# Optimization experiments

Measured on AMD Instinct MI355X. Metric: run time of the kernel, lower is better.

## Reference

```python
import jax, jax.numpy as jnp
import numpy as np

B = 1_000_000  # batch of independent 3-node graphs (trajectory samples)
H = 32         # hidden_channels

# fully-connected 3-node graph with self-loops, deg=3 => D^-1/2 A D^-1/2 = ones(3,3)/3
A_NORM = jnp.full((3, 3), 1.0 / 3.0, dtype=jnp.float32)


def setup_inputs() -> dict:
    key = jax.random.key(0)
    ks = jax.random.split(key, 8)
    return {
        "x":    jax.random.normal(ks[0], (B, 3, 4), jnp.float32),
        "W1":   jax.random.normal(ks[1], (4, H), jnp.float32) * 0.3,
        "b1":   jnp.zeros((H,), jnp.float32),
        "W2":   jax.random.normal(ks[2], (H, H), jnp.float32) * 0.15,
        "b2":   jnp.zeros((H,), jnp.float32),
        "W3":   jax.random.normal(ks[3], (H, H), jnp.float32) * 0.15,
        "b3":   jnp.zeros((H,), jnp.float32),
        "W4":   jax.random.normal(ks[4], (H, H), jnp.float32) * 0.15,
        "b4":   jnp.zeros((H,), jnp.float32),
        "linW": jax.random.normal(ks[5], (1, 3), jnp.float32) * 0.3,  # torch Linear(3,1) weight [out,in]
        "linb": jnp.zeros((1,), jnp.float32),
    }


def _gcn(h, W, b):
    # GCNLayer (eval mode: dropout is identity):
    #   linear -> symmetric-normalized sum over neighbors (= mean over all 3 nodes) -> bias -> softplus
    # h: [B, 3, Fin] -> [B, 3, Fout]
    return jax.nn.softplus(jnp.einsum('ij,bjf->bif', A_NORM, h @ W) + b)


def reference(x, W1, b1, W2, b2, W3, b3, W4, b4, linW, linb):
    h = _gcn(x, W1, b1)   # [B,3,32]
    h = _gcn(h, W2, b2)
    h = _gcn(h, W3, b3)
    h = _gcn(h, W4, b4)   # [B,3,32]
    h = jnp.swapaxes(h, -2, -1)      # [B,32,3]
    return h @ linW.T + linb         # [B,32,1]
```

## Files before the change

kernel.cpp:

```cpp
#include <hip/hip_runtime.h>
#include <math.h>


#define BLK 256
#define ROWSTRIDE 36

using short8 = __attribute__((ext_vector_type(8))) short;
using f32x4  = __attribute__((ext_vector_type(4))) float;

__device__ __forceinline__ short8 as_s8(uint4 u) { return __builtin_bit_cast(short8, u); }

__device__ __forceinline__ float softplus_fast(float a) {
    return __logf(1.0f + __expf(a));
}

__device__ __forceinline__ unsigned pack_hilo(float a) {
    unsigned u  = __float_as_uint(a);
    unsigned hb = (u + 0x7fffu + ((u >> 16) & 1u)) & 0xffff0000u;
    float    r  = a - __uint_as_float(hb);
    unsigned lo = __float_as_uint(r) >> 16;
    return hb | lo;
}

__global__ __launch_bounds__(BLK, 3) void gnn_mfma(
    const float* __restrict__ x,
    const float* __restrict__ W1, const float* __restrict__ b1,
    const float* __restrict__ W2, const float* __restrict__ b2,
    const float* __restrict__ W3, const float* __restrict__ b3,
    const float* __restrict__ W4, const float* __restrict__ b4,
    const float* __restrict__ linW, const float* __restrict__ linb,
    float* __restrict__ out, int nB)
{
    __shared__ unsigned lds[4 * 64 * ROWSTRIDE];

    const int tid  = threadIdx.x;
    const int wid  = tid >> 6;
    const int lane = tid & 63;
    const int q    = lane >> 4;
    const int l16  = lane & 15;

    unsigned* myLds = lds + wid * (64 * ROWSTRIDE);
    const int sbase = blockIdx.x * BLK + wid * 64;

    const int b0 = sbase + lane;
    float xm0 = 0.f, xm1 = 0.f, xm2 = 0.f, xm3 = 0.f;
    if (b0 < nB) {
        const float4* xp = (const float4*)(x + (size_t)b0 * 12);
        float4 n0 = xp[0], n1 = xp[1], n2 = xp[2];
        const float inv3 = 1.0f / 3.0f;
        xm0 = (n0.x + n1.x + n2.x) * inv3;
        xm1 = (n0.y + n1.y + n2.y) * inv3;
        xm2 = (n0.z + n1.z + n2.z) * inv3;
        xm3 = (n0.w + n1.w + n2.w) * inv3;
    }

    {
        unsigned vp[32];
        #pragma unroll
        for (int f = 0; f < 32; ++f) {
            float a = b1[f];
            a = fmaf(xm0, W1[f],      a);
            a = fmaf(xm1, W1[32 + f], a);
            a = fmaf(xm2, W1[64 + f], a);
            a = fmaf(xm3, W1[96 + f], a);
            vp[f] = pack_hilo(softplus_fast(a));
        }
        uint4* rowp = (uint4*)(myLds + lane * ROWSTRIDE);
        #pragma unroll
        for (int d = 0; d < 8; ++d)
            rowp[d] = make_uint4(vp[4*d], vp[4*d+1], vp[4*d+2], vp[4*d+3]);
    }

    const float* Ws[3] = { W2, W3, W4 };
    const float* bs[3] = { b2, b3, b4 };
    const float s_lin = linW[0] + linW[1] + linW[2];
    const float lb    = linb[0];

    #pragma unroll
    for (int layer = 0; layer < 3; ++layer) {
        const float* __restrict__ W  = Ws[layer];
        const float* __restrict__ bL = bs[layer];

        uint4 bhi[2], blo[2];
        #pragma unroll
        for (int nt = 0; nt < 2; ++nt) {
            float w[8];
            #pragma unroll
            for (int j = 0; j < 8; ++j)
                w[j] = W[(q * 8 + j) * 32 + nt * 16 + l16];
            #pragma unroll
            for (int d = 0; d < 4; ++d) {
                unsigned u0  = __float_as_uint(w[2*d]);
                unsigned hb0 = (u0 + 0x7fffu + ((u0 >> 16) & 1u)) & 0xffff0000u;
                float    r0  = w[2*d] - __uint_as_float(hb0);
                unsigned lo0 = __float_as_uint(r0) >> 16;
                unsigned u1  = __float_as_uint(w[2*d+1]);
                unsigned hb1 = (u1 + 0x7fffu + ((u1 >> 16) & 1u)) & 0xffff0000u;
                float    r1  = w[2*d+1] - __uint_as_float(hb1);
                unsigned lo1 = __float_as_uint(r1) >> 16;
                (&bhi[nt].x)[d] = hb1 | (hb0 >> 16);
                (&blo[nt].x)[d] = (lo1 << 16) | lo0;
            }
        }
        const float bias_v0 = bL[l16];
        const float bias_v1 = bL[16 + l16];

        uint4 ahi[4], alo[4];
        #pragma unroll
        for (int mt = 0; mt < 4; ++mt) {
            const uint4* ap = (const uint4*)(myLds + (mt * 16 + l16) * ROWSTRIDE + q * 8);
            uint4 pA = ap[0], pB = ap[1];
            unsigned p[8] = { pA.x, pA.y, pA.z, pA.w, pB.x, pB.y, pB.z, pB.w };
            #pragma unroll
            for (int d = 0; d < 4; ++d) {
                (&ahi[mt].x)[d] = __builtin_amdgcn_perm(p[2*d+1], p[2*d], 0x07060302u);
                (&alo[mt].x)[d] = __builtin_amdgcn_perm(p[2*d+1], p[2*d], 0x05040100u);
            }
        }

        f32x4 acc[4][2];
        #pragma unroll
        for (int mt = 0; mt < 4; ++mt)
            #pragma unroll
            for (int nt = 0; nt < 2; ++nt) {
                f32x4 c = { 0.f, 0.f, 0.f, 0.f };
                c = __builtin_amdgcn_mfma_f32_16x16x32_bf16(as_s8(ahi[mt]), as_s8(bhi[nt]), c, 0, 0, 0);
                c = __builtin_amdgcn_mfma_f32_16x16x32_bf16(as_s8(ahi[mt]), as_s8(blo[nt]), c, 0, 0, 0);
                c = __builtin_amdgcn_mfma_f32_16x16x32_bf16(as_s8(alo[mt]), as_s8(bhi[nt]), c, 0, 0, 0);
                acc[mt][nt] = c;
            }

        if (layer < 2) {
            #pragma unroll
            for (int mt = 0; mt < 4; ++mt)
                #pragma unroll
                for (int nt = 0; nt < 2; ++nt)
                    #pragma unroll
                    for (int r = 0; r < 4; ++r) {
                        float a = acc[mt][nt][r] + (nt ? bias_v1 : bias_v0);
                        int srow = mt * 16 + q * 4 + r;
                        myLds[srow * ROWSTRIDE + nt * 16 + l16] = pack_hilo(softplus_fast(a));
                    }
        } else {
            #pragma unroll
            for (int mt = 0; mt < 4; ++mt)
                #pragma unroll
                for (int nt = 0; nt < 2; ++nt)
                    #pragma unroll
                    for (int r = 0; r < 4; ++r) {
                        float a = acc[mt][nt][r] + (nt ? bias_v1 : bias_v0);
                        float v = softplus_fast(a);
                        int srow = mt * 16 + q * 4 + r;
                        int samp = sbase + srow;
                        if (samp < nB)
                            out[(size_t)samp * 32 + nt * 16 + l16] = fmaf(s_lin, v, lb);
                    }
        }
    }
}

extern "C" void kernel_launch(void* const* d_in, const int* in_sizes, int n_in,
                              void* d_out, int out_size, void* d_ws, size_t ws_size,
                              hipStream_t stream) {
    const float* x    = (const float*)d_in[0];
    const float* W1   = (const float*)d_in[1];
    const float* b1   = (const float*)d_in[2];
    const float* W2   = (const float*)d_in[3];
    const float* b2   = (const float*)d_in[4];
    const float* W3   = (const float*)d_in[5];
    const float* b3   = (const float*)d_in[6];
    const float* W4   = (const float*)d_in[7];
    const float* b4   = (const float*)d_in[8];
    const float* linW = (const float*)d_in[9];
    const float* linb = (const float*)d_in[10];
    float* out = (float*)d_out;

    const int nB   = in_sizes[0] / 12;
    const int grid = (nB + BLK - 1) / BLK;
    gnn_mfma<<<grid, BLK, 0, stream>>>(x, W1, b1, W2, b2, W3, b3, W4, b4,
                                       linW, linb, out, nB);
}
```

Baseline: 234.3 us.

## Store activations as plain bf16 and compute softplus in log2 domain

```diff
diff --git a/kernel.cpp b/kernel.cpp
--- a/kernel.cpp
+++ b/kernel.cpp
@@ -3,26 +3,29 @@
 
 
 #define BLK 256
-#define ROWSTRIDE 36
+#define RS  20
+
+#define LOG2E 1.44269504088896340736f
+#define LN2   0.69314718055994530942f
 
 using short8 = __attribute__((ext_vector_type(8))) short;
 using f32x4  = __attribute__((ext_vector_type(4))) float;
 
 __device__ __forceinline__ short8 as_s8(uint4 u) { return __builtin_bit_cast(short8, u); }
 
-__device__ __forceinline__ float softplus_fast(float a) {
-    return __logf(1.0f + __expf(a));
+__device__ __forceinline__ unsigned bf16_rne(float a) {
+    unsigned u = __float_as_uint(a);
+    return (u + 0x7fffu + ((u >> 16) & 1u)) >> 16;
+}
+__device__ __forceinline__ unsigned pack_bf16x2(float lo, float hi) {
+    return bf16_rne(lo) | (bf16_rne(hi) << 16);
 }
 
-__device__ __forceinline__ unsigned pack_hilo(float a) {
-    unsigned u  = __float_as_uint(a);
-    unsigned hb = (u + 0x7fffu + ((u >> 16) & 1u)) & 0xffff0000u;
-    float    r  = a - __uint_as_float(hb);
-    unsigned lo = __float_as_uint(r) >> 16;
-    return hb | lo;
+__device__ __forceinline__ float softplus_log2(float t) {
+    return __builtin_amdgcn_logf(1.0f + __builtin_amdgcn_exp2f(t));
 }
 
-__global__ __launch_bounds__(BLK, 3) void gnn_mfma(
+__global__ __launch_bounds__(BLK, 3) void gnn_mfma4(
     const float* __restrict__ x,
     const float* __restrict__ W1, const float* __restrict__ b1,
     const float* __restrict__ W2, const float* __restrict__ b2,
@@ -31,7 +34,7 @@
     const float* __restrict__ linW, const float* __restrict__ linb,
     float* __restrict__ out, int nB)
 {
-    __shared__ unsigned lds[4 * 64 * ROWSTRIDE];
+    __shared__ unsigned lds[4 * 64 * RS];
 
     const int tid  = threadIdx.x;
     const int wid  = tid >> 6;
@@ -39,7 +42,7 @@
     const int q    = lane >> 4;
     const int l16  = lane & 15;
 
-    unsigned* myLds = lds + wid * (64 * ROWSTRIDE);
+    unsigned* myLds = lds + wid * (64 * RS);
     const int sbase = blockIdx.x * BLK + wid * 64;
 
     const int b0 = sbase + lane;
@@ -47,34 +50,36 @@
     if (b0 < nB) {
         const float4* xp = (const float4*)(x + (size_t)b0 * 12);
         float4 n0 = xp[0], n1 = xp[1], n2 = xp[2];
-        const float inv3 = 1.0f / 3.0f;
-        xm0 = (n0.x + n1.x + n2.x) * inv3;
-        xm1 = (n0.y + n1.y + n2.y) * inv3;
-        xm2 = (n0.z + n1.z + n2.z) * inv3;
-        xm3 = (n0.w + n1.w + n2.w) * inv3;
+        const float k = LOG2E / 3.0f;
+        xm0 = (n0.x + n1.x + n2.x) * k;
+        xm1 = (n0.y + n1.y + n2.y) * k;
+        xm2 = (n0.z + n1.z + n2.z) * k;
+        xm3 = (n0.w + n1.w + n2.w) * k;
     }
-
     {
-        unsigned vp[32];
+        float u[32];
         #pragma unroll
         for (int f = 0; f < 32; ++f) {
-            float a = b1[f];
-            a = fmaf(xm0, W1[f],      a);
-            a = fmaf(xm1, W1[32 + f], a);
-            a = fmaf(xm2, W1[64 + f], a);
-            a = fmaf(xm3, W1[96 + f], a);
-            vp[f] = pack_hilo(softplus_fast(a));
+            float t = LOG2E * b1[f];
+            t = fmaf(xm0, W1[f],      t);
+            t = fmaf(xm1, W1[32 + f], t);
+            t = fmaf(xm2, W1[64 + f], t);
+            t = fmaf(xm3, W1[96 + f], t);
+            u[f] = softplus_log2(t);
         }
-        uint4* rowp = (uint4*)(myLds + lane * ROWSTRIDE);
+        uint4* rowp = (uint4*)(myLds + lane * RS);
         #pragma unroll
-        for (int d = 0; d < 8; ++d)
-            rowp[d] = make_uint4(vp[4*d], vp[4*d+1], vp[4*d+2], vp[4*d+3]);
+        for (int d = 0; d < 4; ++d)
+            rowp[d] = make_uint4(pack_bf16x2(u[4*d + 0], u[4*d + 16]),
+                                 pack_bf16x2(u[4*d + 1], u[4*d + 17]),
+                                 pack_bf16x2(u[4*d + 2], u[4*d + 18]),
+                                 pack_bf16x2(u[4*d + 3], u[4*d + 19]));
     }
 
     const float* Ws[3] = { W2, W3, W4 };
     const float* bs[3] = { b2, b3, b4 };
-    const float s_lin = linW[0] + linW[1] + linW[2];
-    const float lb    = linb[0];
+    const float s_lin_ln2 = (linW[0] + linW[1] + linW[2]) * LN2;
+    const float lb        = linb[0];
 
     #pragma unroll
     for (int layer = 0; layer < 3; ++layer) {
@@ -84,39 +89,24 @@
         uint4 bhi[2], blo[2];
         #pragma unroll
         for (int nt = 0; nt < 2; ++nt) {
-            float w[8];
-            #pragma unroll
-            for (int j = 0; j < 8; ++j)
-                w[j] = W[(q * 8 + j) * 32 + nt * 16 + l16];
             #pragma unroll
             for (int d = 0; d < 4; ++d) {
-                unsigned u0  = __float_as_uint(w[2*d]);
-                unsigned hb0 = (u0 + 0x7fffu + ((u0 >> 16) & 1u)) & 0xffff0000u;
-                float    r0  = w[2*d] - __uint_as_float(hb0);
-                unsigned lo0 = __float_as_uint(r0) >> 16;
-                unsigned u1  = __float_as_uint(w[2*d+1]);
-                unsigned hb1 = (u1 + 0x7fffu + ((u1 >> 16) & 1u)) & 0xffff0000u;
-                float    r1  = w[2*d+1] - __uint_as_float(hb1);
-                unsigned lo1 = __float_as_uint(r1) >> 16;
-                (&bhi[nt].x)[d] = hb1 | (hb0 >> 16);
-                (&blo[nt].x)[d] = (lo1 << 16) | lo0;
+                float w0 = W[(q * 4 + d) * 32      + nt * 16 + l16];
+                float w1 = W[(q * 4 + d + 16) * 32 + nt * 16 + l16];
+                unsigned h0 = bf16_rne(w0), h1 = bf16_rne(w1);
+                float w0h = __uint_as_float(h0 << 16);
+                float w1h = __uint_as_float(h1 << 16);
+                (&bhi[nt].x)[d] = h0 | (h1 << 16);
+                (&blo[nt].x)[d] = pack_bf16x2(w0 - w0h, w1 - w1h);
             }
         }
-        const float bias_v0 = bL[l16];
-        const float bias_v1 = bL[16 + l16];
+        const float bias0 = LOG2E * bL[l16];
+        const float bias1 = LOG2E * bL[16 + l16];
 
-        uint4 ahi[4], alo[4];
+        uint4 afr[4];
         #pragma unroll
-        for (int mt = 0; mt < 4; ++mt) {
-            const uint4* ap = (const uint4*)(myLds + (mt * 16 + l16) * ROWSTRIDE + q * 8);
-            uint4 pA = ap[0], pB = ap[1];
-            unsigned p[8] = { pA.x, pA.y, pA.z, pA.w, pB.x, pB.y, pB.z, pB.w };
-            #pragma unroll
-            for (int d = 0; d < 4; ++d) {
-                (&ahi[mt].x)[d] = __builtin_amdgcn_perm(p[2*d+1], p[2*d], 0x07060302u);
-                (&alo[mt].x)[d] = __builtin_amdgcn_perm(p[2*d+1], p[2*d], 0x05040100u);
-            }
-        }
+        for (int mt = 0; mt < 4; ++mt)
+            afr[mt] = *(const uint4*)(myLds + (mt * 16 + l16) * RS + q * 4);
 
         f32x4 acc[4][2];
         #pragma unroll
@@ -124,9 +114,8 @@
             #pragma unroll
             for (int nt = 0; nt < 2; ++nt) {
                 f32x4 c = { 0.f, 0.f, 0.f, 0.f };
-                c = __builtin_amdgcn_mfma_f32_16x16x32_bf16(as_s8(ahi[mt]), as_s8(bhi[nt]), c, 0, 0, 0);
-                c = __builtin_amdgcn_mfma_f32_16x16x32_bf16(as_s8(ahi[mt]), as_s8(blo[nt]), c, 0, 0, 0);
-                c = __builtin_amdgcn_mfma_f32_16x16x32_bf16(as_s8(alo[mt]), as_s8(bhi[nt]), c, 0, 0, 0);
+                c = __builtin_amdgcn_mfma_f32_16x16x32_bf16(as_s8(afr[mt]), as_s8(blo[nt]), c, 0, 0, 0);
+                c = __builtin_amdgcn_mfma_f32_16x16x32_bf16(as_s8(afr[mt]), as_s8(bhi[nt]), c, 0, 0, 0);
                 acc[mt][nt] = c;
             }
 
@@ -134,27 +123,25 @@
             #pragma unroll
             for (int mt = 0; mt < 4; ++mt)
                 #pragma unroll
-                for (int nt = 0; nt < 2; ++nt)
-                    #pragma unroll
-                    for (int r = 0; r < 4; ++r) {
-                        float a = acc[mt][nt][r] + (nt ? bias_v1 : bias_v0);
-                        int srow = mt * 16 + q * 4 + r;
-                        myLds[srow * ROWSTRIDE + nt * 16 + l16] = pack_hilo(softplus_fast(a));
-                    }
+                for (int r = 0; r < 4; ++r) {
+                    float v0 = softplus_log2(acc[mt][0][r] + bias0);
+                    float v1 = softplus_log2(acc[mt][1][r] + bias1);
+                    myLds[(mt * 16 + q * 4 + r) * RS + l16] = pack_bf16x2(v0, v1);
+                }
         } else {
             #pragma unroll
             for (int mt = 0; mt < 4; ++mt)
                 #pragma unroll
-                for (int nt = 0; nt < 2; ++nt)
-                    #pragma unroll
-                    for (int r = 0; r < 4; ++r) {
-                        float a = acc[mt][nt][r] + (nt ? bias_v1 : bias_v0);
-                        float v = softplus_fast(a);
-                        int srow = mt * 16 + q * 4 + r;
-                        int samp = sbase + srow;
-                        if (samp < nB)
-                            out[(size_t)samp * 32 + nt * 16 + l16] = fmaf(s_lin, v, lb);
+                for (int r = 0; r < 4; ++r) {
+                    int samp = sbase + mt * 16 + q * 4 + r;
+                    if (samp < nB) {
+                        float v0 = softplus_log2(acc[mt][0][r] + bias0);
+                        float v1 = softplus_log2(acc[mt][1][r] + bias1);
+                        float* op = out + (size_t)samp * 32;
+                        op[l16]      = fmaf(s_lin_ln2, v0, lb);
+                        op[16 + l16] = fmaf(s_lin_ln2, v1, lb);
                     }
+                }
         }
     }
 }
@@ -177,6 +164,6 @@
 
     const int nB   = in_sizes[0] / 12;
     const int grid = (nB + BLK - 1) / BLK;
-    gnn_mfma<<<grid, BLK, 0, stream>>>(x, W1, b1, W2, b2, W3, b3, W4, b4,
-                                       linW, linb, out, nB);
+    gnn_mfma4<<<grid, BLK, 0, stream>>>(x, W1, b1, W2, b2, W3, b3, W4, b4,
+                                        linW, linb, out, nB);
 }
```

Result: faster. 198.7 us (-15.2%).
